# Kernel optimization log

Hardware: AMD Instinct MI355X
Metric: run time of the kernel (lower is better)

## Reference

```python
import jax, jax.numpy as jnp
import numpy as np

B, H, W, C = 32, 56, 56, 192
WS, SHIFT, NH = 7, 3, 6
HD = C // NH
N = WS * WS
NW = (H // WS) * (W // WS)
SCALE = HD ** -0.5
EPS = 1e-5


def _layer_norm(x, g, b):
    mu = jnp.mean(x, axis=-1, keepdims=True)
    var = jnp.mean(jnp.square(x - mu), axis=-1, keepdims=True)
    return (x - mu) * jax.lax.rsqrt(var + EPS) * g + b


def _relative_position_index():
    coords = np.stack(np.meshgrid(np.arange(WS), np.arange(WS), indexing='ij'))  # [2,ws,ws]
    coords = coords.reshape(2, -1)                                               # [2,N]
    rel = coords[:, :, None] - coords[:, None, :]                                # [2,N,N]
    rel = rel.transpose(1, 2, 0).astype(np.int64)
    rel[..., 0] += WS - 1
    rel[..., 1] += WS - 1
    rel[..., 0] *= 2 * WS - 1
    return jnp.asarray(rel.sum(-1))  # [N,N]


def _attn_mask():
    img = np.zeros((H, W), dtype=np.float32)
    cnt = 0
    slices = (slice(0, -WS), slice(-WS, -SHIFT), slice(-SHIFT, None))
    for hs in slices:
        for ws_ in slices:
            img[hs, ws_] = cnt
            cnt += 1
    mw = img.reshape(H // WS, WS, W // WS, WS).transpose(0, 2, 1, 3).reshape(-1, N)  # [nW,N]
    diff = mw[:, :, None] - mw[:, None, :]
    return jnp.asarray(np.where(diff != 0, -100.0, 0.0).astype(np.float32))  # [nW,N,N]


REL_IDX = _relative_position_index()
ATTN_MASK = _attn_mask()


def setup_inputs() -> dict:
    key = jax.random.key(0)
    ks = jax.random.split(key, 16)
    s = 0.02
    return {
        'x': jax.random.normal(ks[0], (B, H * W, C), jnp.float32),
        'ln1_g': jnp.ones((C,), jnp.float32),
        'ln1_b': jnp.zeros((C,), jnp.float32),
        'qkv_w': jax.random.normal(ks[1], (3 * C, C), jnp.float32) * s,
        'qkv_b': jnp.zeros((3 * C,), jnp.float32),
        'proj_w': jax.random.normal(ks[2], (C, C), jnp.float32) * s,
        'proj_b': jnp.zeros((C,), jnp.float32),
        'rpb_table': jax.random.normal(ks[3], ((2 * WS - 1) ** 2, NH), jnp.float32) * s,
        'ln2_g': jnp.ones((C,), jnp.float32),
        'ln2_b': jnp.zeros((C,), jnp.float32),
        'fc1_w': jax.random.normal(ks[4], (4 * C, C), jnp.float32) * s,
        'fc1_b': jnp.zeros((4 * C,), jnp.float32),
        'fc2_w': jax.random.normal(ks[5], (C, 4 * C), jnp.float32) * s,
        'fc2_b': jnp.zeros((C,), jnp.float32),
    }


def reference(x, ln1_g, ln1_b, qkv_w, qkv_b, proj_w, proj_b, rpb_table,
              ln2_g, ln2_b, fc1_w, fc1_b, fc2_w, fc2_b):
    shortcut = x
    h = _layer_norm(x, ln1_g, ln1_b).reshape(B, H, W, C)
    # cyclic shift
    h = jnp.roll(h, (-SHIFT, -SHIFT), axis=(1, 2))
    # window partition -> [B*nW, N, C]
    h = h.reshape(B, H // WS, WS, W // WS, WS, C).transpose(0, 1, 3, 2, 4, 5)
    h = h.reshape(B * NW, N, C)
    # qkv
    qkv = h @ qkv_w.T + qkv_b                                   # [Bn,N,3C]
    qkv = qkv.reshape(B * NW, N, 3, NH, HD).transpose(2, 0, 3, 1, 4)
    q, k, v = qkv[0], qkv[1], qkv[2]                             # [Bn,nh,N,hd]
    attn = jnp.einsum('bhnd,bhmd->bhnm', q * SCALE, k)           # [Bn,nh,N,N]
    # relative position bias
    bias = rpb_table[REL_IDX.reshape(-1)].reshape(N, N, NH).transpose(2, 0, 1)
    attn = attn + bias[None]
    # shift mask
    attn = attn.reshape(B, NW, NH, N, N) + ATTN_MASK[None, :, None]
    attn = jax.nn.softmax(attn.reshape(B * NW, NH, N, N), axis=-1)
    h = jnp.einsum('bhnm,bhmd->bhnd', attn, v)                   # [Bn,nh,N,hd]
    h = h.transpose(0, 2, 1, 3).reshape(B * NW, N, C)
    h = h @ proj_w.T + proj_b
    # window reverse + reverse shift
    h = h.reshape(B, H // WS, W // WS, WS, WS, C).transpose(0, 1, 3, 2, 4, 5)
    h = h.reshape(B, H, W, C)
    h = jnp.roll(h, (SHIFT, SHIFT), axis=(1, 2)).reshape(B, H * W, C)
    x = shortcut + h
    # MLP
    m = _layer_norm(x, ln2_g, ln2_b)
    m = jax.nn.gelu(m @ fc1_w.T + fc1_b, approximate=False)
    m = m @ fc2_w.T + fc2_b
    return x + m
```

## Files before the change

### kernel.cpp

```cpp
#include <hip/hip_runtime.h>
#include <hip/hip_bf16.h>
#include <cstdint>
#include <cstddef>

typedef __hip_bfloat16 bf16;
using f32x4  = __attribute__((ext_vector_type(4))) float;
using bf16x8 = __attribute__((ext_vector_type(8))) short;

#define DEVI __device__ __forceinline__

DEVI int reg3(int u) { return (u < 49) ? 0 : ((u < 53) ? 1 : 2); }

DEVI unsigned short f2bu(float v) {
  bf16 b = __float2bfloat16(v);
  return *reinterpret_cast<unsigned short*>(&b);
}

DEVI float gelu_f(float v) {
  const float y = 0.7978845608028654f * (v + 0.044715f * v * v * v);
  const float e = __expf(2.0f * y);
  const float th = 1.0f - 2.0f / (e + 1.0f);
  return 0.5f * v * (1.0f + th);
}

DEVI void gload_lds16(const void* g, void* l) {
  __builtin_amdgcn_global_load_lds(
      (const __attribute__((address_space(1))) unsigned int*)g,
      (__attribute__((address_space(3))) unsigned int*)l, 16, 0, 0);
}

__global__ __launch_bounds__(256) void cvt_kernel(const float* __restrict__ src,
                                                  bf16* __restrict__ dst, int n)
{
  const int i = blockIdx.x * 256 + threadIdx.x;
  if (i < n) dst[i] = __float2bfloat16(src[i]);
}

template<bool PERM>
__global__ __launch_bounds__(256) void ln_kernel(const float* __restrict__ x,
                                                 const float* __restrict__ gw,
                                                 const float* __restrict__ bw,
                                                 bf16* __restrict__ out,
                                                 int grow0)
{
  const int lane = threadIdx.x & 63;
  const int ridx = blockIdx.x * 4 + (threadIdx.x >> 6);
  size_t src;
  if (PERM) {
    const int g   = grow0 + ridx;
    const int wid = g / 49;
    const int nn  = g - wid * 49;
    const int b_  = wid >> 6, wim = wid & 63;
    const int wy  = wim >> 3, wx = wim & 7;
    const int ny  = nn / 7,  nx = nn - (nn / 7) * 7;
    int i = wy * 7 + ny + 3; if (i >= 56) i -= 56;
    int j = wx * 7 + nx + 3; if (j >= 56) j -= 56;
    src = (size_t)(b_ * 3136 + i * 56 + j);
  } else {
    src = (size_t)ridx;
  }
  const float* xr = x + src * 192;
  float v0 = xr[lane];
  float v1 = xr[lane + 64];
  float v2 = xr[lane + 128];
  float s = v0 + v1 + v2;
#pragma unroll
  for (int off = 32; off > 0; off >>= 1) s += __shfl_xor(s, off);
  const float mu = s * (1.0f / 192.0f);
  const float d0 = v0 - mu, d1 = v1 - mu, d2 = v2 - mu;
  float vs = d0 * d0 + d1 * d1 + d2 * d2;
#pragma unroll
  for (int off = 32; off > 0; off >>= 1) vs += __shfl_xor(vs, off);
  const float rstd = rsqrtf(vs * (1.0f / 192.0f) + 1e-5f);
  bf16* orow = out + (size_t)ridx * 192;
  orow[lane]       = __float2bfloat16(d0 * rstd * gw[lane]       + bw[lane]);
  orow[lane + 64]  = __float2bfloat16(d1 * rstd * gw[lane + 64]  + bw[lane + 64]);
  orow[lane + 128] = __float2bfloat16(d2 * rstd * gw[lane + 128] + bw[lane + 128]);
}

template<int MODE>
__global__ __launch_bounds__(512) void pgemm_kernel(const bf16* __restrict__ A,
                                                    const bf16* __restrict__ Bt,
                                                    const float* __restrict__ bias,
                                                    const float* __restrict__ resid,
                                                    void* __restrict__ outv,
                                                    int N, int grow0, int MT)
{
  __shared__ short Bp[192 * 192];
  __shared__ short La[2][64 * 192];
  const int tid  = threadIdx.x;
  const int lane = tid & 63;
  const int w    = tid >> 6;
  const int wm   = (w >> 2) * 32;
  const int wn   = (w & 3) * 48;
  const int np   = blockIdx.x;
  const int n0   = np * 192;
  const int G    = gridDim.y;
  const int g    = blockIdx.y;
  const int kq   = lane >> 4;

#pragma unroll
  for (int i = 0; i < 9; i++) {
    const int chunk = w * 9 + i;
    const int idx = chunk * 64 + lane;
    const int row = idx / 24;
    const int seg = idx - row * 24;
    const int ksrc = (seg * 8) ^ ((row & 7) << 3);
    gload_lds16(Bt + (size_t)(n0 + row) * 192 + ksrc, Bp + chunk * 512);
  }

  auto stageA = [&](int buf, int mt) {
    const int m0 = mt * 64;
#pragma unroll
    for (int i = 0; i < 3; i++) {
      const int chunk = w * 3 + i;
      const int idx = chunk * 64 + lane;
      const int row = idx / 24;
      const int seg = idx - row * 24;
      const int ksrc = (seg * 8) ^ ((row & 7) << 3);
      gload_lds16(A + (size_t)(m0 + row) * 192 + ksrc, &La[buf][0] + chunk * 512);
    }
  };

  int buf = 0;
  stageA(0, g < MT ? g : 0);
  __syncthreads();

  for (int mt = g; mt < MT; mt += G) {
    if (mt + G < MT) stageA(buf ^ 1, mt + G);
    const char* LA = (const char*)&La[buf][0];

    f32x4 acc[2][3];
#pragma unroll
    for (int i = 0; i < 2; i++)
#pragma unroll
      for (int j = 0; j < 3; j++) acc[i][j] = (f32x4){0.f, 0.f, 0.f, 0.f};

#pragma unroll
    for (int kk = 0; kk < 6; kk++) {
      const int q = kk * 64 + (kq << 4);
      bf16x8 af[2], bg[3];
#pragma unroll
      for (int mf = 0; mf < 2; mf++) {
        const int ar = wm + mf * 16 + (lane & 15);
        af[mf] = *(const bf16x8*)(LA + ar * 384 + (q ^ ((ar & 7) << 4)));
      }
#pragma unroll
      for (int nf = 0; nf < 3; nf++) {
        const int br = wn + nf * 16 + (lane & 15);
        bg[nf] = *(const bf16x8*)((const char*)Bp + br * 384 + (q ^ ((br & 7) << 4)));
      }
#pragma unroll
      for (int mf = 0; mf < 2; mf++)
#pragma unroll
        for (int nf = 0; nf < 3; nf++)
          acc[mf][nf] = __builtin_amdgcn_mfma_f32_16x16x32_bf16(af[mf], bg[nf], acc[mf][nf], 0, 0, 0);
    }

    const int m0 = mt * 64;
    float bv[3];
    int ncol[3];
#pragma unroll
    for (int nf = 0; nf < 3; nf++) {
      ncol[nf] = n0 + wn + nf * 16 + (lane & 15);
      bv[nf]   = bias[ncol[nf]];
    }
#pragma unroll
    for (int mf = 0; mf < 2; mf++) {
#pragma unroll
      for (int r = 0; r < 4; r++) {
        const int m = m0 + wm + mf * 16 + ((lane >> 4) << 2) + r;
        if constexpr (MODE == 1) {
          const int gm  = grow0 + m;
          const int wid = gm / 49;
          const int nn  = gm - wid * 49;
          const int b_  = wid >> 6, wim = wid & 63;
          const int wy  = wim >> 3, wx = wim & 7;
          const int ny  = nn / 7, nx = nn - (nn / 7) * 7;
          int i = wy * 7 + ny + 3; if (i >= 56) i -= 56;
          int j = wx * 7 + nx + 3; if (j >= 56) j -= 56;
          const size_t t = (size_t)(b_ * 3136 + i * 56 + j) * 192;
          float* O = (float*)outv;
#pragma unroll
          for (int nf = 0; nf < 3; nf++)
            O[t + ncol[nf]] = acc[mf][nf][r] + bv[nf] + resid[t + ncol[nf]];
        } else {
          bf16* O = (bf16*)outv + (size_t)m * N;
#pragma unroll
          for (int nf = 0; nf < 3; nf++) {
            float v = acc[mf][nf][r] + bv[nf];
            if constexpr (MODE == 2) v = gelu_f(v);
            O[ncol[nf]] = __float2bfloat16(v);
          }
        }
      }
    }
    __syncthreads();
    buf ^= 1;
  }
}

template<int MODE>
__global__ __launch_bounds__(512, 4) void gemm_kernel(const bf16* __restrict__ A,
                                                      const bf16* __restrict__ Bt,
                                                      const float* __restrict__ bias,
                                                      const float* __restrict__ resid,
                                                      void* __restrict__ outv,
                                                      int N, int K, int grow0)
{
  __shared__ short lds[2][128 * 64 + 192 * 64];
  const int tid  = threadIdx.x;
  const int lane = tid & 63;
  const int w    = tid >> 6;
  const int wm   = (w >> 2) * 64;
  const int wn   = (w & 3) * 48;
  const int m0   = blockIdx.y * 128;
  const int n0   = blockIdx.x * 192;
  const int lrow = lane >> 3;
  const int lseg = lane & 7;
  const int ksw  = (lseg * 8) ^ (lrow << 3);

  f32x4 acc[4][3];
#pragma unroll
  for (int i = 0; i < 4; i++)
#pragma unroll
    for (int j = 0; j < 3; j++) acc[i][j] = (f32x4){0.f, 0.f, 0.f, 0.f};

  const int nk = K >> 6;

  auto issue = [&](int buf, int kt) {
    const int k0 = kt << 6;
    short* LA = &lds[buf][0];
    short* LB = &lds[buf][128 * 64];
#pragma unroll
    for (int i = 0; i < 2; i++) {
      const int chunk = w * 2 + i;
      gload_lds16(A + (size_t)(m0 + chunk * 8 + lrow) * K + (k0 + ksw), LA + chunk * 512);
    }
#pragma unroll
    for (int i = 0; i < 3; i++) {
      const int chunk = w * 3 + i;
      gload_lds16(Bt + (size_t)(n0 + chunk * 8 + lrow) * K + (k0 + ksw), LB + chunk * 512);
    }
  };

  issue(0, 0);
  __syncthreads();

  for (int kt = 0; kt < nk; kt++) {
    const int buf = kt & 1;
    if (kt + 1 < nk) issue(buf ^ 1, kt + 1);
    const char* LA = (const char*)&lds[buf][0];
    const char* LB = (const char*)&lds[buf][128 * 64];
#pragma unroll
    for (int kk = 0; kk < 2; kk++) {
      bf16x8 af[4], bg[3];
#pragma unroll
      for (int mf = 0; mf < 4; mf++) {
        const int row = wm + mf * 16 + (lane & 15);
        const int kb  = (kk * 64 + ((lane >> 4) << 4)) ^ ((row & 7) << 4);
        af[mf] = *(const bf16x8*)(LA + row * 128 + kb);
      }
#pragma unroll
      for (int nf = 0; nf < 3; nf++) {
        const int row = wn + nf * 16 + (lane & 15);
        const int kb  = (kk * 64 + ((lane >> 4) << 4)) ^ ((row & 7) << 4);
        bg[nf] = *(const bf16x8*)(LB + row * 128 + kb);
      }
#pragma unroll
      for (int mf = 0; mf < 4; mf++)
#pragma unroll
        for (int nf = 0; nf < 3; nf++)
          acc[mf][nf] = __builtin_amdgcn_mfma_f32_16x16x32_bf16(af[mf], bg[nf], acc[mf][nf], 0, 0, 0);
    }
    __syncthreads();
  }

  float bv[3];
  int ncol[3];
#pragma unroll
  for (int nf = 0; nf < 3; nf++) {
    ncol[nf] = n0 + wn + nf * 16 + (lane & 15);
    bv[nf]   = bias[ncol[nf]];
  }
#pragma unroll
  for (int mf = 0; mf < 4; mf++) {
#pragma unroll
    for (int r = 0; r < 4; r++) {
      const int m = m0 + wm + mf * 16 + ((lane >> 4) << 2) + r;
      float* O = (float*)outv + (size_t)m * N;
#pragma unroll
      for (int nf = 0; nf < 3; nf++)
        O[ncol[nf]] = acc[mf][nf][r] + bv[nf] + O[ncol[nf]];
    }
  }
}

__global__ __launch_bounds__(64) void attn_kernel(const bf16* __restrict__ qkv,
                                                  const float* __restrict__ rpb,
                                                  bf16* __restrict__ aout)
{
  __shared__ unsigned short Vt[32 * 64];
  __shared__ unsigned short Pl[64 * 64];
  __shared__ float Bl[169];
  const int lane = threadIdx.x;
  const int wid  = blockIdx.x;
  const int h    = blockIdx.y;
  const unsigned short* qkvu = (const unsigned short*)qkv;
  const size_t base = (size_t)wid * 49 * 576 + h * 32;

#pragma unroll
  for (int i = 0; i < 3; i++) {
    const int idx = lane + 64 * i;
    if (idx < 169) Bl[idx] = rpb[idx * 6 + h];
  }
#pragma unroll
  for (int i = 0; i < 8; i++)
    ((unsigned long long*)Vt)[lane + 64 * i] = 0ull;

#pragma unroll
  for (int it = 0; it < 7; it++) {
    const int idx = lane + 64 * it;
    if (idx < 392) {
      const int n  = idx >> 3;
      const int d0 = (idx & 7) * 4;
      ushort4 v = *(const ushort4*)(qkvu + base + (size_t)n * 576 + 384 + d0);
      Vt[(d0 + 0) * 64 + (n ^ (((d0 + 0) & 7) << 3))] = v.x;
      Vt[(d0 + 1) * 64 + (n ^ (((d0 + 1) & 7) << 3))] = v.y;
      Vt[(d0 + 2) * 64 + (n ^ (((d0 + 2) & 7) << 3))] = v.z;
      Vt[(d0 + 3) * 64 + (n ^ (((d0 + 3) & 7) << 3))] = v.w;
    }
  }

  bf16x8 qf[4], kf[4];
#pragma unroll
  for (int t = 0; t < 4; t++) {
    int rq = (lane & 15) + t * 16; if (rq > 48) rq = 48;
    qf[t] = *(const bf16x8*)(qkvu + base + (size_t)rq * 576 + ((lane >> 4) * 8));
    kf[t] = *(const bf16x8*)(qkvu + base + (size_t)rq * 576 + 192 + ((lane >> 4) * 8));
  }

  f32x4 s[4][4];
#pragma unroll
  for (int mt = 0; mt < 4; mt++)
#pragma unroll
    for (int nt = 0; nt < 4; nt++)
      s[mt][nt] = __builtin_amdgcn_mfma_f32_16x16x32_bf16(qf[mt], kf[nt],
                    (f32x4){0.f, 0.f, 0.f, 0.f}, 0, 0, 0);

  const int wim = wid & 63;
  const int wy = wim >> 3, wx = wim & 7;
  int labn[4], ch[4], cw[4];
  bool cval[4];
#pragma unroll
  for (int nt = 0; nt < 4; nt++) {
    const int C = (lane & 15) + nt * 16;
    cval[nt] = (C < 49);
    const int cc = cval[nt] ? C : 48;
    ch[nt] = cc / 7; cw[nt] = cc - ch[nt] * 7;
    labn[nt] = reg3(wy * 7 + ch[nt]) * 3 + reg3(wx * 7 + cw[nt]);
  }

#pragma unroll
  for (int mt = 0; mt < 4; mt++) {
    f32x4 rm, sm, inv;
#pragma unroll
    for (int r = 0; r < 4; r++) {
      int R = mt * 16 + ((lane >> 4) << 2) + r; if (R > 48) R = 48;
      const int mh = R / 7, mw = R - (R / 7) * 7;
      const int labm = reg3(wy * 7 + mh) * 3 + reg3(wx * 7 + mw);
#pragma unroll
      for (int nt = 0; nt < 4; nt++) {
        float sv = s[mt][nt][r] * 0.1767766953f
                 + Bl[(mh - ch[nt] + 6) * 13 + (mw - cw[nt] + 6)];
        if (labn[nt] != labm) sv -= 100.f;
        if (!cval[nt]) sv = -3e38f;
        s[mt][nt][r] = sv;
      }
      rm[r] = fmaxf(fmaxf(s[mt][0][r], s[mt][1][r]), fmaxf(s[mt][2][r], s[mt][3][r]));
    }
#pragma unroll
    for (int mk = 1; mk < 16; mk <<= 1)
#pragma unroll
      for (int r = 0; r < 4; r++) rm[r] = fmaxf(rm[r], __shfl_xor(rm[r], mk));
#pragma unroll
    for (int r = 0; r < 4; r++) {
      float acc = 0.f;
#pragma unroll
      for (int nt = 0; nt < 4; nt++) {
        const float p = __expf(s[mt][nt][r] - rm[r]);
        s[mt][nt][r] = p;
        acc += p;
      }
      sm[r] = acc;
    }
#pragma unroll
    for (int mk = 1; mk < 16; mk <<= 1)
#pragma unroll
      for (int r = 0; r < 4; r++) sm[r] += __shfl_xor(sm[r], mk);
#pragma unroll
    for (int r = 0; r < 4; r++) inv[r] = 1.0f / sm[r];
#pragma unroll
    for (int nt = 0; nt < 4; nt++)
#pragma unroll
      for (int r = 0; r < 4; r++) {
        const int R = mt * 16 + ((lane >> 4) << 2) + r;
        const int C = (lane & 15) + nt * 16;
        Pl[R * 64 + (C ^ ((R & 7) << 3))] = f2bu(s[mt][nt][r] * inv[r]);
      }
  }

  f32x4 o[4][2];
#pragma unroll
  for (int mt = 0; mt < 4; mt++)
#pragma unroll
    for (int n2 = 0; n2 < 2; n2++) o[mt][n2] = (f32x4){0.f, 0.f, 0.f, 0.f};
#pragma unroll
  for (int kk = 0; kk < 2; kk++) {
    const int kb = kk * 64 + ((lane >> 4) << 4);
    bf16x8 vb[2];
#pragma unroll
    for (int n2 = 0; n2 < 2; n2++) {
      const int d = (lane & 15) + n2 * 16;
      vb[n2] = *(const bf16x8*)((const char*)Vt + d * 128 + (kb ^ ((d & 7) << 4)));
    }
#pragma unroll
    for (int mt = 0; mt < 4; mt++) {
      const int R = (lane & 15) + mt * 16;
      const bf16x8 pa = *(const bf16x8*)((const char*)Pl + R * 128 + (kb ^ ((R & 7) << 4)));
#pragma unroll
      for (int n2 = 0; n2 < 2; n2++)
        o[mt][n2] = __builtin_amdgcn_mfma_f32_16x16x32_bf16(pa, vb[n2], o[mt][n2], 0, 0, 0);
    }
  }

#pragma unroll
  for (int mt = 0; mt < 4; mt++)
#pragma unroll
    for (int r = 0; r < 4; r++) {
      const int R = mt * 16 + ((lane >> 4) << 2) + r;
      if (R < 49) {
        bf16* orow = aout + (size_t)(wid * 49 + R) * 192 + h * 32;
#pragma unroll
        for (int n2 = 0; n2 < 2; n2++)
          orow[n2 * 16 + (lane & 15)] = __float2bfloat16(o[mt][n2][r]);
      }
    }
}

extern "C" void kernel_launch(void* const* d_in, const int* in_sizes, int n_in,
                              void* d_out, int out_size, void* d_ws, size_t ws_size,
                              hipStream_t stream)
{
  (void)in_sizes; (void)n_in; (void)out_size;
  const float* x     = (const float*)d_in[0];
  const float* ln1g  = (const float*)d_in[1];
  const float* ln1b  = (const float*)d_in[2];
  const float* qkvw  = (const float*)d_in[3];
  const float* qkvb  = (const float*)d_in[4];
  const float* projw = (const float*)d_in[5];
  const float* projb = (const float*)d_in[6];
  const float* rpb   = (const float*)d_in[7];
  const float* ln2g  = (const float*)d_in[8];
  const float* ln2b  = (const float*)d_in[9];
  const float* fc1w  = (const float*)d_in[10];
  const float* fc1b  = (const float*)d_in[11];
  const float* fc2w  = (const float*)d_in[12];
  const float* fc2b  = (const float*)d_in[13];
  float* out = (float*)d_out;
  char* ws   = (char*)d_ws;

  bf16* wqkv = (bf16*)(ws);
  bf16* wproj = (bf16*)(ws + 221184);
  bf16* wfc1 = (bf16*)(ws + 294912);
  bf16* wfc2 = (bf16*)(ws + 589824);
  cvt_kernel<<<dim3(432), dim3(256), 0, stream>>>(qkvw, wqkv, 110592);
  cvt_kernel<<<dim3(144), dim3(256), 0, stream>>>(projw, wproj, 36864);
  cvt_kernel<<<dim3(576), dim3(256), 0, stream>>>(fc1w, wfc1, 147456);
  cvt_kernel<<<dim3(576), dim3(256), 0, stream>>>(fc2w, wfc2, 147456);

  char* cws = ws + 884736;
  const size_t avail = (ws_size > 884736ull) ? ws_size - 884736ull : 0;

  int Bc = 32;
  while (Bc > 2 && (size_t)Bc * 4816896ull > avail) Bc >>= 1;
  const int nb = 32 / Bc;
  bf16* qkv_c  = (bf16*)cws;
  bf16* hwin_c = (bf16*)(cws + (size_t)Bc * 3612672ull);

  for (int c = 0; c < nb; c++) {
    const int R0 = c * Bc * 3136;
    const int Mc = Bc * 3136;
    const int MT = Mc / 64;
    ln_kernel<true><<<dim3(Mc / 4), dim3(256), 0, stream>>>(x, ln1g, ln1b, hwin_c, R0);
    pgemm_kernel<0><<<dim3(3, 170), dim3(512), 0, stream>>>(hwin_c, wqkv, qkvb, nullptr, qkv_c, 576, 0, MT);
    attn_kernel<<<dim3(Bc * 64, 6), dim3(64), 0, stream>>>(qkv_c, rpb, hwin_c);
    pgemm_kernel<1><<<dim3(1, 256), dim3(512), 0, stream>>>(hwin_c, wproj, projb, x, out, 192, R0, MT);
  }

  int Rc = 100352;
  while (Rc > 6272 && (size_t)Rc * 1920ull > avail) Rc >>= 1;
  bf16* ln2_c = (bf16*)cws;
  bf16* a1_c  = (bf16*)(cws + (size_t)Rc * 384ull);

  for (int r0 = 0; r0 < 100352; r0 += Rc) {
    ln_kernel<false><<<dim3(Rc / 4), dim3(256), 0, stream>>>(out + (size_t)r0 * 192, ln2g, ln2b, ln2_c, 0);
    pgemm_kernel<2><<<dim3(4, 128), dim3(512), 0, stream>>>(ln2_c, wfc1, fc1b, nullptr, a1_c, 768, 0, Rc / 64);
    gemm_kernel<3><<<dim3(1, Rc / 128), dim3(512), 0, stream>>>(a1_c, wfc2, fc2b, nullptr, out + (size_t)r0 * 192, 192, 768, 0);
  }
}
```

Before: 374.9 us.

## Rework GEMM pipelining with explicit vmcnt waits and resize persistent grids

The persistent GEMM now prefetches the next A tile after the MFMA loop rather than before it. It uses explicit s_waitcnt vmcnt plus a raw s_barrier in place of __syncthreads, so the epilogue stores overlap the next tile's loads. The fc2 GEMM uses the same vmcnt-based barrier scheme. Grid sizes for the qkv and fc1 persistent GEMMs are also changed (qkv grid made smaller, fc1 grid halved), trading parallelism for more reuse of the resident weight tile. The hardcoded vmcnt counts depend on exact load counts and risk races if the compiler reorders or merges memory operations.

```diff
diff --git a/kernel.cpp b/kernel.cpp
--- a/kernel.cpp
+++ b/kernel.cpp
@@ -8,6 +8,7 @@
 using bf16x8 = __attribute__((ext_vector_type(8))) short;
 
 #define DEVI __device__ __forceinline__
+#define WAITVM(N) asm volatile("s_waitcnt vmcnt(" #N ")" ::: "memory")
 
 DEVI int reg3(int u) { return (u < 49) ? 0 : ((u < 53) ? 1 : 2); }
 
@@ -93,11 +94,18 @@
   const int w    = tid >> 6;
   const int wm   = (w >> 2) * 32;
   const int wn   = (w & 3) * 48;
-  const int np   = blockIdx.x;
-  const int n0   = np * 192;
+  const int n0   = blockIdx.x * 192;
   const int G    = gridDim.y;
   const int g    = blockIdx.y;
   const int kq   = lane >> 4;
+
+  float bv[3];
+  int ncol[3];
+#pragma unroll
+  for (int nf = 0; nf < 3; nf++) {
+    ncol[nf] = n0 + wn + nf * 16 + (lane & 15);
+    bv[nf]   = bias[ncol[nf]];
+  }
 
 #pragma unroll
   for (int i = 0; i < 9; i++) {
@@ -123,13 +131,14 @@
   };
 
   int buf = 0;
-  stageA(0, g < MT ? g : 0);
+  if (g < MT) stageA(0, g);
   __syncthreads();
 
   for (int mt = g; mt < MT; mt += G) {
-    if (mt + G < MT) stageA(buf ^ 1, mt + G);
+    if constexpr (MODE == 1) { WAITVM(48); } else { WAITVM(24); }
+    __builtin_amdgcn_s_barrier();
+
     const char* LA = (const char*)&La[buf][0];
-
     f32x4 acc[2][3];
 #pragma unroll
     for (int i = 0; i < 2; i++)
@@ -157,14 +166,9 @@
           acc[mf][nf] = __builtin_amdgcn_mfma_f32_16x16x32_bf16(af[mf], bg[nf], acc[mf][nf], 0, 0, 0);
     }
 
+    if (mt + G < MT) stageA(buf ^ 1, mt + G);
+
     const int m0 = mt * 64;
-    float bv[3];
-    int ncol[3];
-#pragma unroll
-    for (int nf = 0; nf < 3; nf++) {
-      ncol[nf] = n0 + wn + nf * 16 + (lane & 15);
-      bv[nf]   = bias[ncol[nf]];
-    }
 #pragma unroll
     for (int mf = 0; mf < 2; mf++) {
 #pragma unroll
@@ -195,18 +199,15 @@
         }
       }
     }
-    __syncthreads();
     buf ^= 1;
   }
 }
 
-template<int MODE>
 __global__ __launch_bounds__(512, 4) void gemm_kernel(const bf16* __restrict__ A,
                                                       const bf16* __restrict__ Bt,
                                                       const float* __restrict__ bias,
-                                                      const float* __restrict__ resid,
                                                       void* __restrict__ outv,
-                                                      int N, int K, int grow0)
+                                                      int N, int K)
 {
   __shared__ short lds[2][128 * 64 + 192 * 64];
   const int tid  = threadIdx.x;
@@ -246,10 +247,16 @@
 
   issue(0, 0);
   __syncthreads();
+  int buf = 0;
 
   for (int kt = 0; kt < nk; kt++) {
-    const int buf = kt & 1;
-    if (kt + 1 < nk) issue(buf ^ 1, kt + 1);
+    if (kt + 1 < nk) {
+      issue(buf ^ 1, kt + 1);
+      WAITVM(5);
+    } else {
+      WAITVM(0);
+    }
+    __builtin_amdgcn_s_barrier();
     const char* LA = (const char*)&lds[buf][0];
     const char* LB = (const char*)&lds[buf][128 * 64];
 #pragma unroll
@@ -273,7 +280,8 @@
         for (int nf = 0; nf < 3; nf++)
           acc[mf][nf] = __builtin_amdgcn_mfma_f32_16x16x32_bf16(af[mf], bg[nf], acc[mf][nf], 0, 0, 0);
     }
-    __syncthreads();
+    __builtin_amdgcn_s_barrier();
+    buf ^= 1;
   }
 
   float bv[3];
@@ -492,10 +500,12 @@
     const int R0 = c * Bc * 3136;
     const int Mc = Bc * 3136;
     const int MT = Mc / 64;
+    const int Gq = (MT < 85) ? MT : 85;
+    const int Gp = (MT < 256) ? MT : 256;
     ln_kernel<true><<<dim3(Mc / 4), dim3(256), 0, stream>>>(x, ln1g, ln1b, hwin_c, R0);
-    pgemm_kernel<0><<<dim3(3, 170), dim3(512), 0, stream>>>(hwin_c, wqkv, qkvb, nullptr, qkv_c, 576, 0, MT);
+    pgemm_kernel<0><<<dim3(3, Gq), dim3(512), 0, stream>>>(hwin_c, wqkv, qkvb, nullptr, qkv_c, 576, 0, MT);
     attn_kernel<<<dim3(Bc * 64, 6), dim3(64), 0, stream>>>(qkv_c, rpb, hwin_c);
-    pgemm_kernel<1><<<dim3(1, 256), dim3(512), 0, stream>>>(hwin_c, wproj, projb, x, out, 192, R0, MT);
+    pgemm_kernel<1><<<dim3(1, Gp), dim3(512), 0, stream>>>(hwin_c, wproj, projb, x, out, 192, R0, MT);
   }
 
   int Rc = 100352;
@@ -504,8 +514,10 @@
   bf16* a1_c  = (bf16*)(cws + (size_t)Rc * 384ull);
 
   for (int r0 = 0; r0 < 100352; r0 += Rc) {
+    const int MT1 = Rc / 64;
+    const int G1  = (MT1 < 64) ? MT1 : 64;
     ln_kernel<false><<<dim3(Rc / 4), dim3(256), 0, stream>>>(out + (size_t)r0 * 192, ln2g, ln2b, ln2_c, 0);
-    pgemm_kernel<2><<<dim3(4, 128), dim3(512), 0, stream>>>(ln2_c, wfc1, fc1b, nullptr, a1_c, 768, 0, Rc / 64);
-    gemm_kernel<3><<<dim3(1, Rc / 128), dim3(512), 0, stream>>>(a1_c, wfc2, fc2b, nullptr, out + (size_t)r0 * 192, 192, 768, 0);
-  }
-}
+    pgemm_kernel<2><<<dim3(4, G1), dim3(512), 0, stream>>>(ln2_c, wfc1, fc1b, nullptr, a1_c, 768, 0, MT1);
+    gemm_kernel<<<dim3(1, Rc / 128), dim3(512), 0, stream>>>(a1_c, wfc2, fc2b, out + (size_t)r0 * 192, 192, 768);
+  }
+}
```

Measured after the change: 354.2 us (median of 2 runs). 5.5% less time.
